# Kernel tuning notes

Hardware: AMD Instinct MI355X
Metric: run time of the kernel (lower is better)

## Reference

```python
import jax, jax.numpy as jnp
import numpy as np

ALPHA = 0.2  # leaky relu negative slope
MASK_VAL = -9e15

def setup_inputs() -> dict:
    key = jax.random.key(0)
    k1, k2, k3, k4, k5 = jax.random.split(key, 5)
    B, N, F = 8, 2048, 256
    x = jax.random.normal(k1, (B, N, F), dtype=jnp.float32)
    adj = jax.random.randint(k2, (B, N, N), 0, 2, dtype=jnp.int32)
    # params scaled down to keep activations in a sane range through 4 layers
    W0 = jax.random.normal(k3, (F, F), dtype=jnp.float32) * 0.05
    Wrest = jax.random.normal(k4, (3, F, F), dtype=jnp.float32) * 0.05
    A = jax.random.normal(k5, (4, 2 * F), dtype=jnp.float32) * 0.05
    return {"x": x, "adj": adj, "W0": W0, "Wrest": Wrest, "A": A}

def _gat_layer(h, adj, W, a):
    # h: [B,N,Fin], W: [Fin,Fout], a: [2*Fout]
    Fout = W.shape[1]
    Wh = jnp.einsum('bnf,fo->bno', h, W)  # [B,N,Fout]
    # a_input @ a decomposes: e[b,i,j] = leakyrelu(a1.Wh_i + a2.Wh_j)
    f1 = Wh @ a[:Fout]   # [B,N]
    f2 = Wh @ a[Fout:]   # [B,N]
    e = jax.nn.leaky_relu(f1[:, :, None] + f2[:, None, :], ALPHA)  # [B,N,N]
    masked = jnp.where(adj > 0, e, jnp.float32(MASK_VAL))
    att = jax.nn.softmax(masked, axis=1)  # NOTE: dim=1 as in the source
    # dropout is identity in eval mode
    return jnp.einsum('bij,bjo->bio', att, Wh)  # concat=False: no elu here

def reference(x, adj, W0, Wrest, A):
    # eval mode: all F.dropout calls are identity
    h = jax.nn.leaky_relu(_gat_layer(x, adj, W0, A[0]), ALPHA)
    for i in range(Wrest.shape[0]):
        h = jax.nn.leaky_relu(_gat_layer(h, adj, Wrest[i], A[i + 1]), ALPHA)
    return h
```

## Files before the change

### kernel.cpp

```cpp
#include <hip/hip_runtime.h>
#include <math.h>

#define BB 8
#define NN 2048
#define FF 256
#define NW 64
#define ALPHA 0.2f
#define L2E 1.44269504f

typedef _Float16 f16x8 __attribute__((ext_vector_type(8)));
typedef __fp16   h16x2 __attribute__((ext_vector_type(2)));
typedef float    f32x4 __attribute__((ext_vector_type(4)));
typedef unsigned long long u64;

__device__ __forceinline__ float lrelu(float x){ return fmaxf(x, ALPHA*x); }

__global__ void pack_prep(const int* __restrict__ adj, u64* __restrict__ packed,
                          const float* __restrict__ x, _Float16* __restrict__ h0,
                          const float* __restrict__ W0, const float* __restrict__ Wrest,
                          _Float16* __restrict__ Wt){
    __shared__ _Float16 Ls[64][66];
    int blk = blockIdx.x, t = threadIdx.x;
    if (blk < 64){
        int lw = blk >> 4, rest = blk & 15;
        int c0 = (rest >> 2)*64, k0 = (rest & 3)*64;
        const float* Win = (lw == 0) ? W0 : (Wrest + (size_t)(lw-1)*FF*FF);
        for (int it = 0; it < 4; ++it){
            int idx = it*256 + t;
            int r = idx >> 4, c4 = (idx & 15)*4;
            float4 v = *(const float4*)&Win[(size_t)(k0 + r)*FF + c0 + c4];
            Ls[c4+0][r] = (_Float16)v.x; Ls[c4+1][r] = (_Float16)v.y;
            Ls[c4+2][r] = (_Float16)v.z; Ls[c4+3][r] = (_Float16)v.w;
        }
        __syncthreads();
        int c = t >> 2, jch = t & 3;
        const unsigned* lp = (const unsigned*)&Ls[c][jch*16];
        int4 o0 = make_int4(lp[0], lp[1], lp[2], lp[3]);
        int4 o1 = make_int4(lp[4], lp[5], lp[6], lp[7]);
        _Float16* dst = Wt + ((size_t)lw*FF + c0 + c)*FF + k0 + jch*16;
        *(int4*)dst = o0;
        *(int4*)(dst + 8) = o1;
    }
    long long idx = (long long)blk*blockDim.x + t;
    long long stride = (long long)gridDim.x*blockDim.x;
    const long long total = (long long)BB*NN*NN;
    for (long long i = idx; i < total; i += stride){
        u64 m = __ballot(adj[i] > 0);
        if ((t & 63) == 0) packed[i >> 6] = m;
    }
    const long long nx4 = (long long)BB*NN*FF/4;
    for (long long i = idx; i < nx4; i += stride){
        float4 v = ((const float4*)x)[i];
        union { _Float16 h[4]; u64 u; } cv;
        cv.h[0] = (_Float16)v.x; cv.h[1] = (_Float16)v.y;
        cv.h[2] = (_Float16)v.z; cv.h[3] = (_Float16)v.w;
        ((u64*)h0)[i] = cv.u;
    }
}

__global__ __launch_bounds__(512,2) void gemm_hw(const _Float16* __restrict__ hin,
        const _Float16* __restrict__ Wt, const float* __restrict__ Avec,
        char* __restrict__ Bp, float* __restrict__ f1, float* __restrict__ f2){
    __shared__ float fred[2][64][4];
    int t = threadIdx.x, l = t & 63, wid = t >> 6;
    int wr = wid >> 2, wc = wid & 3;
    int lg = l >> 4, lr = l & 15;
    size_t i0 = (size_t)blockIdx.x * 64;
    f32x4 acc[2][4] = {};
    for (int k0 = 0; k0 < FF; k0 += 32){
        f16x8 a[2], bf[4];
        #pragma unroll
        for (int m = 0; m < 2; ++m){
            int4 v = *(const int4*)&hin[(i0 + wr*32 + m*16 + lr)*FF + k0 + lg*8];
            a[m] = *(f16x8*)&v;
        }
        #pragma unroll
        for (int n = 0; n < 4; ++n){
            int4 v = *(const int4*)&Wt[(size_t)(wc*64 + n*16 + lr)*FF + k0 + lg*8];
            bf[n] = *(f16x8*)&v;
        }
        #pragma unroll
        for (int m = 0; m < 2; ++m)
            #pragma unroll
            for (int n = 0; n < 4; ++n)
                acc[m][n] = __builtin_amdgcn_mfma_f32_16x16x32_f16(a[m], bf[n], acc[m][n], 0, 0, 0);
    }
    int b   = (int)(i0 >> 11);
    int i0l = (int)(i0 & (NN-1));
    char* Bpb = Bp + ((size_t)b << 20);
    int kb  = (i0l >> 5) + wr;
    #pragma unroll
    for (int m = 0; m < 2; ++m){
        int lgp = m*2 + (lg >> 1);
        int eb  = (lg & 1)*4;
        #pragma unroll
        for (int n = 0; n < 4; ++n){
            union { _Float16 h[4]; u64 u; } pk;
            pk.h[0] = (_Float16)acc[m][n][0]; pk.h[1] = (_Float16)acc[m][n][1];
            pk.h[2] = (_Float16)acc[m][n][2]; pk.h[3] = (_Float16)acc[m][n][3];
            int c16 = wc*4 + n;
            size_t off = ((size_t)(c16*64 + kb) << 10) + (size_t)((lgp*16 + lr)*16 + eb*2);
            *(u64*)(Bpb + off) = pk.u;
        }
    }
    float a1v[4], a2v[4];
    #pragma unroll
    for (int n = 0; n < 4; ++n){
        a1v[n] = Avec[wc*64 + n*16 + lr];
        a2v[n] = Avec[FF + wc*64 + n*16 + lr];
    }
    #pragma unroll
    for (int m = 0; m < 2; ++m){
        #pragma unroll
        for (int q = 0; q < 4; ++q){
            float p1 = 0.f, p2 = 0.f;
            #pragma unroll
            for (int n = 0; n < 4; ++n){
                float v = acc[m][n][q];
                p1 = fmaf(v, a1v[n], p1);
                p2 = fmaf(v, a2v[n], p2);
            }
            #pragma unroll
            for (int msk = 1; msk < 16; msk <<= 1){
                p1 += __shfl_xor(p1, msk);
                p2 += __shfl_xor(p2, msk);
            }
            if (lr == 0){
                fred[0][wr*32 + m*16 + lg*4 + q][wc] = p1;
                fred[1][wr*32 + m*16 + lg*4 + q][wc] = p2;
            }
        }
    }
    __syncthreads();
    if (t < 128){
        int row = t & 63, f = t >> 6;
        float v = fred[f][row][0] + fred[f][row][1] + fred[f][row][2] + fred[f][row][3];
        (f ? f2 : f1)[i0 + row] = v * L2E;
    }
}

__global__ __launch_bounds__(512,2) void spass_g(const u64* __restrict__ packed,
        const float* __restrict__ f1, const float* __restrict__ f2, float* __restrict__ g){
    __shared__ float sred[128][33];
    __shared__ float sred2[8][33];
    int blk = blockIdx.x, t = threadIdx.x;
    int b2 = blk >> 6, jt = blk & 63;
    const unsigned* pb32 = (const unsigned*)(packed + (size_t)b2*NN*(NW/2));
    const float* f1b = f1 + b2*NN;
    int jg = t & 3, ic = t >> 2;
    int j0 = jt*32 + jg*8;
    float f2v[8];
    *(float4*)&f2v[0] = *(const float4*)&f2[b2*NN + j0];
    *(float4*)&f2v[4] = *(const float4*)&f2[b2*NN + j0 + 4];
    int wi = jt, sh = jg*8;
    float acc[8] = {};
    #pragma unroll 4
    for (int ii = 0; ii < 16; ++ii){
        int i = ic*16 + ii;
        unsigned w = pb32[(size_t)i*NW + wi] >> sh;
        float f1v = f1b[i];
        #pragma unroll
        for (int e = 0; e < 8; ++e){
            float xv = f1v + f2v[e];
            float p = __builtin_amdgcn_exp2f(fmaxf(xv, ALPHA*xv));
            acc[e] += ((w >> e) & 1u) ? p : 0.f;
        }
    }
    #pragma unroll
    for (int e = 0; e < 8; ++e) sred[ic][jg*8 + e] = acc[e];
    __syncthreads();
    if (t < 256){
        int j = t & 31, part = t >> 5;
        float s = 0.f;
        #pragma unroll
        for (int k = 0; k < 16; ++k) s += sred[part*16 + k][j];
        sred2[part][j] = s;
    }
    __syncthreads();
    if (t < 32){
        float s = 0.f;
        #pragma unroll
        for (int p = 0; p < 8; ++p) s += sred2[p][t];
        g[b2*NN + jt*32 + t] = -__builtin_amdgcn_logf(s);
    }
}

__global__ __launch_bounds__(512,2) void gemm_att(const char* __restrict__ Bp,
        const u64* __restrict__ packed64, const float* __restrict__ f1,
        const float* __restrict__ f2, const float* __restrict__ g,
        _Float16* __restrict__ hnext, float* __restrict__ out, int last){
    __shared__ char Ps0[8192];
    __shared__ char Ps1[8192];
    __shared__ float FG[2][NN];
    int t = threadIdx.x, l = t & 63, wid = t >> 6;
    int lg = l >> 4, lr = l & 15;
    int b  = blockIdx.x & 7;
    int i0 = (blockIdx.x >> 3) * 64;
    const char* Bpw = Bp + ((size_t)b << 20) + ((size_t)(wid*2*64) << 10) + (size_t)(l << 4);
    const u64* pb = packed64 + (size_t)b*NN*(NW/2);
    ((float4*)&FG[0][0])[t] = ((const float4*)(f2 + b*NN))[t];
    ((float4*)&FG[1][0])[t] = ((const float4*)(g  + b*NN))[t];
    int prow = t >> 3, pch = t & 7;
    float f1v = f1[b*NN + i0 + prow];
    const u64* prowp = pb + (size_t)(i0 + prow)*(NW/2);
    int pso = prow*128 + ((pch << 4) ^ ((prow & 7) << 4));

    int4 brega[4], bregb[4];
    float fv[8], gv[8];
    unsigned w8;
    f32x4 acc[4][2] = {};

    #define LOADB(reg_, ks_) do{                                                       \
        _Pragma("unroll")                                                              \
        for (int n = 0; n < 2; ++n)                                                    \
          _Pragma("unroll")                                                            \
          for (int kk = 0; kk < 2; ++kk)                                               \
            reg_[n*2+kk] = *(const int4*)(Bpw + (((size_t)(n*64 + (ks_)*2 + kk)) << 10)); \
    }while(0)

    #define LOADP(ks_) do{                                                             \
        w8 = (unsigned)(prowp[ks_] >> (pch*8)) & 0xffu;                                \
        int jb_ = (ks_)*64 + pch*8;                                                    \
        *(float4*)&fv[0] = *(const float4*)&FG[0][jb_];                                \
        *(float4*)&fv[4] = *(const float4*)&FG[0][jb_+4];                              \
        *(float4*)&gv[0] = *(const float4*)&FG[1][jb_];                                \
        *(float4*)&gv[4] = *(const float4*)&FG[1][jb_+4];                              \
    }while(0)

    #define WRITEP(pbase_) do{                                                         \
        float pf_[8];                                                                  \
        _Pragma("unroll")                                                              \
        for (int e = 0; e < 8; ++e){                                                   \
            float xv_ = f1v + fv[e];                                                   \
            float p_ = __builtin_amdgcn_exp2f(fmaxf(xv_, ALPHA*xv_) + gv[e]);          \
            pf_[e] = ((w8 >> e) & 1u) ? p_ : 0.f;                                      \
        }                                                                              \
        union { h16x2 h2[4]; f16x8 v8; } pu_;                                          \
        pu_.h2[0] = __builtin_amdgcn_cvt_pkrtz(pf_[0], pf_[1]);                        \
        pu_.h2[1] = __builtin_amdgcn_cvt_pkrtz(pf_[2], pf_[3]);                        \
        pu_.h2[2] = __builtin_amdgcn_cvt_pkrtz(pf_[4], pf_[5]);                        \
        pu_.h2[3] = __builtin_amdgcn_cvt_pkrtz(pf_[6], pf_[7]);                        \
        *(f16x8*)((pbase_) + pso) = pu_.v8;                                            \
    }while(0)

    #define MFMA_STEP(reg_, pbase_) do{                                                \
        f16x8 pa_[4][2];                                                               \
        _Pragma("unroll")                                                              \
        for (int m = 0; m < 4; ++m){                                                   \
            int row_ = m*16 + lr;                                                      \
            _Pragma("unroll")                                                          \
            for (int kk = 0; kk < 2; ++kk)                                             \
                pa_[m][kk] = *(const f16x8*)((pbase_) + row_*128 + (((kk*4 + lg) << 4) ^ ((row_ & 7) << 4))); \
        }                                                                              \
        _Pragma("unroll")                                                              \
        for (int n = 0; n < 2; ++n)                                                    \
          _Pragma("unroll")                                                            \
          for (int kk = 0; kk < 2; ++kk){                                              \
            f16x8 bf_ = *(const f16x8*)&reg_[n*2+kk];                                  \
            _Pragma("unroll")                                                          \
            for (int m = 0; m < 4; ++m)                                                \
                acc[m][n] = __builtin_amdgcn_mfma_f32_16x16x32_f16(pa_[m][kk], bf_, acc[m][n], 0, 0, 0); \
          }                                                                            \
    }while(0)

    LOADB(brega, 0);
    __syncthreads();
    LOADP(0); WRITEP(Ps0);
    __syncthreads();
    for (int ks2 = 0; ks2 < 16; ++ks2){
        int s = 2*ks2;
        LOADB(bregb, s+1); LOADP(s+1);
        MFMA_STEP(brega, Ps0);
        WRITEP(Ps1);
        __syncthreads();
        if (ks2 < 15){ LOADB(brega, s+2); LOADP(s+2); }
        MFMA_STEP(bregb, Ps1);
        if (ks2 < 15){ WRITEP(Ps0); __syncthreads(); }
    }
    #undef LOADB
    #undef LOADP
    #undef WRITEP
    #undef MFMA_STEP

    size_t obase = (size_t)b*NN*FF;
    #pragma unroll
    for (int m = 0; m < 4; ++m){
        #pragma unroll
        for (int q = 0; q < 4; ++q){
            size_t row = i0 + m*16 + lg*4 + q;
            #pragma unroll
            for (int n = 0; n < 2; ++n){
                int col = wid*32 + n*16 + lr;
                float v = lrelu(acc[m][n][q]);
                if (last) out[obase + row*FF + col] = v;
                else      hnext[obase + row*FF + col] = (_Float16)v;
            }
        }
    }
}

extern "C" void kernel_launch(void* const* d_in, const int* in_sizes, int n_in,
                              void* d_out, int out_size, void* d_ws, size_t ws_size,
                              hipStream_t stream){
    const float* x     = (const float*)d_in[0];
    const int*   adj   = (const int*)  d_in[1];
    const float* W0    = (const float*)d_in[2];
    const float* Wrest = (const float*)d_in[3];
    const float* A     = (const float*)d_in[4];
    float* out = (float*)d_out;

    char* ws = (char*)d_ws;
    size_t off = 0;
    auto carve = [&](size_t bytes) -> void* {
        void* p = ws + off;
        off += (bytes + 255) & ~(size_t)255;
        return p;
    };
    u64*      packed = (u64*)     carve((size_t)BB*NN*NN/8);
    _Float16* hA     = (_Float16*)carve((size_t)BB*NN*FF*2);
    _Float16* hB     = (_Float16*)carve((size_t)BB*NN*FF*2);
    char*     Bp     = (char*)    carve((size_t)BB*NN*FF*2);
    _Float16* Wt     = (_Float16*)carve((size_t)4*FF*FF*2);
    float*    f1     = (float*)   carve((size_t)BB*NN*4);
    float*    f2     = (float*)   carve((size_t)BB*NN*4);
    float*    g      = (float*)   carve((size_t)BB*NN*4);

    pack_prep<<<2048, 256, 0, stream>>>(adj, packed, x, hA, W0, Wrest, Wt);

    _Float16* bufs[2] = {hA, hB};
    const _Float16* hin = hA;
    for (int layer = 0; layer < 4; ++layer){
        const float* Al = A + (size_t)layer*2*FF;
        gemm_hw<<<256, 512, 0, stream>>>(hin, Wt + (size_t)layer*FF*FF, Al, Bp, f1, f2);
        spass_g<<<512, 512, 0, stream>>>(packed, f1, f2, g);
        int last = (layer == 3);
        _Float16* hnext = bufs[(layer + 1) & 1];
        gemm_att<<<256, 512, 0, stream>>>(Bp, packed, f1, f2, g, hnext, out, last);
        hin = hnext;
    }
}
```

Baseline: 239.6 us.

## Split gemm_hw across column halves and double gemm_att k-step per barrier

```diff
diff --git a/kernel.cpp b/kernel.cpp
--- a/kernel.cpp
+++ b/kernel.cpp
@@ -7,6 +7,7 @@
 #define NW 64
 #define ALPHA 0.2f
 #define L2E 1.44269504f
+#define BBNN (BB*NN)
 
 typedef _Float16 f16x8 __attribute__((ext_vector_type(8)));
 typedef __fp16   h16x2 __attribute__((ext_vector_type(2)));
@@ -60,29 +61,30 @@
 
 __global__ __launch_bounds__(512,2) void gemm_hw(const _Float16* __restrict__ hin,
         const _Float16* __restrict__ Wt, const float* __restrict__ Avec,
-        char* __restrict__ Bp, float* __restrict__ f1, float* __restrict__ f2){
+        char* __restrict__ Bp, float* __restrict__ f1p, float* __restrict__ f2p){
     __shared__ float fred[2][64][4];
     int t = threadIdx.x, l = t & 63, wid = t >> 6;
     int wr = wid >> 2, wc = wid & 3;
     int lg = l >> 4, lr = l & 15;
-    size_t i0 = (size_t)blockIdx.x * 64;
-    f32x4 acc[2][4] = {};
+    size_t i0 = (size_t)(blockIdx.x >> 1) * 64;
+    int chalf = blockIdx.x & 1, c0 = chalf * 128;
+    f32x4 acc[2][2] = {};
     for (int k0 = 0; k0 < FF; k0 += 32){
-        f16x8 a[2], bf[4];
+        f16x8 a[2], bf[2];
         #pragma unroll
         for (int m = 0; m < 2; ++m){
             int4 v = *(const int4*)&hin[(i0 + wr*32 + m*16 + lr)*FF + k0 + lg*8];
             a[m] = *(f16x8*)&v;
         }
         #pragma unroll
-        for (int n = 0; n < 4; ++n){
-            int4 v = *(const int4*)&Wt[(size_t)(wc*64 + n*16 + lr)*FF + k0 + lg*8];
+        for (int n = 0; n < 2; ++n){
+            int4 v = *(const int4*)&Wt[(size_t)(c0 + wc*32 + n*16 + lr)*FF + k0 + lg*8];
             bf[n] = *(f16x8*)&v;
         }
         #pragma unroll
         for (int m = 0; m < 2; ++m)
             #pragma unroll
-            for (int n = 0; n < 4; ++n)
+            for (int n = 0; n < 2; ++n)
                 acc[m][n] = __builtin_amdgcn_mfma_f32_16x16x32_f16(a[m], bf[n], acc[m][n], 0, 0, 0);
     }
     int b   = (int)(i0 >> 11);
@@ -94,20 +96,20 @@
         int lgp = m*2 + (lg >> 1);
         int eb  = (lg & 1)*4;
         #pragma unroll
-        for (int n = 0; n < 4; ++n){
+        for (int n = 0; n < 2; ++n){
             union { _Float16 h[4]; u64 u; } pk;
             pk.h[0] = (_Float16)acc[m][n][0]; pk.h[1] = (_Float16)acc[m][n][1];
             pk.h[2] = (_Float16)acc[m][n][2]; pk.h[3] = (_Float16)acc[m][n][3];
-            int c16 = wc*4 + n;
+            int c16 = chalf*8 + wc*2 + n;
             size_t off = ((size_t)(c16*64 + kb) << 10) + (size_t)((lgp*16 + lr)*16 + eb*2);
             *(u64*)(Bpb + off) = pk.u;
         }
     }
-    float a1v[4], a2v[4];
-    #pragma unroll
-    for (int n = 0; n < 4; ++n){
-        a1v[n] = Avec[wc*64 + n*16 + lr];
-        a2v[n] = Avec[FF + wc*64 + n*16 + lr];
+    float a1v[2], a2v[2];
+    #pragma unroll
+    for (int n = 0; n < 2; ++n){
+        a1v[n] = Avec[c0 + wc*32 + n*16 + lr];
+        a2v[n] = Avec[FF + c0 + wc*32 + n*16 + lr];
     }
     #pragma unroll
     for (int m = 0; m < 2; ++m){
@@ -115,7 +117,7 @@
         for (int q = 0; q < 4; ++q){
             float p1 = 0.f, p2 = 0.f;
             #pragma unroll
-            for (int n = 0; n < 4; ++n){
+            for (int n = 0; n < 2; ++n){
                 float v = acc[m][n][q];
                 p1 = fmaf(v, a1v[n], p1);
                 p2 = fmaf(v, a2v[n], p2);
@@ -135,30 +137,37 @@
     if (t < 128){
         int row = t & 63, f = t >> 6;
         float v = fred[f][row][0] + fred[f][row][1] + fred[f][row][2] + fred[f][row][3];
-        (f ? f2 : f1)[i0 + row] = v * L2E;
+        (f ? f2p : f1p)[chalf*BBNN + i0 + row] = v * L2E;
     }
 }
 
 __global__ __launch_bounds__(512,2) void spass_g(const u64* __restrict__ packed,
-        const float* __restrict__ f1, const float* __restrict__ f2, float* __restrict__ g){
+        const float* __restrict__ f1p, const float* __restrict__ f2p, float* __restrict__ g){
     __shared__ float sred[128][33];
     __shared__ float sred2[8][33];
     int blk = blockIdx.x, t = threadIdx.x;
     int b2 = blk >> 6, jt = blk & 63;
     const unsigned* pb32 = (const unsigned*)(packed + (size_t)b2*NN*(NW/2));
-    const float* f1b = f1 + b2*NN;
+    const float* f1b0 = f1p + b2*NN;
+    const float* f1b1 = f1p + BBNN + b2*NN;
     int jg = t & 3, ic = t >> 2;
     int j0 = jt*32 + jg*8;
     float f2v[8];
-    *(float4*)&f2v[0] = *(const float4*)&f2[b2*NN + j0];
-    *(float4*)&f2v[4] = *(const float4*)&f2[b2*NN + j0 + 4];
+    {
+        float4 a0 = *(const float4*)&f2p[b2*NN + j0];
+        float4 a1 = *(const float4*)&f2p[b2*NN + j0 + 4];
+        float4 b0 = *(const float4*)&f2p[BBNN + b2*NN + j0];
+        float4 b1 = *(const float4*)&f2p[BBNN + b2*NN + j0 + 4];
+        f2v[0]=a0.x+b0.x; f2v[1]=a0.y+b0.y; f2v[2]=a0.z+b0.z; f2v[3]=a0.w+b0.w;
+        f2v[4]=a1.x+b1.x; f2v[5]=a1.y+b1.y; f2v[6]=a1.z+b1.z; f2v[7]=a1.w+b1.w;
+    }
     int wi = jt, sh = jg*8;
     float acc[8] = {};
     #pragma unroll 4
     for (int ii = 0; ii < 16; ++ii){
         int i = ic*16 + ii;
         unsigned w = pb32[(size_t)i*NW + wi] >> sh;
-        float f1v = f1b[i];
+        float f1v = f1b0[i] + f1b1[i];
         #pragma unroll
         for (int e = 0; e < 8; ++e){
             float xv = f1v + f2v[e];
@@ -186,11 +195,11 @@
 }
 
 __global__ __launch_bounds__(512,2) void gemm_att(const char* __restrict__ Bp,
-        const u64* __restrict__ packed64, const float* __restrict__ f1,
-        const float* __restrict__ f2, const float* __restrict__ g,
+        const u64* __restrict__ packed64, const float* __restrict__ f1p,
+        const float* __restrict__ f2p, const float* __restrict__ g,
         _Float16* __restrict__ hnext, float* __restrict__ out, int last){
-    __shared__ char Ps0[8192];
-    __shared__ char Ps1[8192];
+    __shared__ char Ps0[16384];
+    __shared__ char Ps1[16384];
     __shared__ float FG[2][NN];
     int t = threadIdx.x, l = t & 63, wid = t >> 6;
     int lg = l >> 4, lr = l & 15;
@@ -198,68 +207,92 @@
     int i0 = (blockIdx.x >> 3) * 64;
     const char* Bpw = Bp + ((size_t)b << 20) + ((size_t)(wid*2*64) << 10) + (size_t)(l << 4);
     const u64* pb = packed64 + (size_t)b*NN*(NW/2);
-    ((float4*)&FG[0][0])[t] = ((const float4*)(f2 + b*NN))[t];
-    ((float4*)&FG[1][0])[t] = ((const float4*)(g  + b*NN))[t];
+    {
+        float4 a = ((const float4*)(f2p + b*NN))[t];
+        float4 c = ((const float4*)(f2p + BBNN + b*NN))[t];
+        float4 s; s.x=a.x+c.x; s.y=a.y+c.y; s.z=a.z+c.z; s.w=a.w+c.w;
+        ((float4*)&FG[0][0])[t] = s;
+        ((float4*)&FG[1][0])[t] = ((const float4*)(g + b*NN))[t];
+    }
     int prow = t >> 3, pch = t & 7;
-    float f1v = f1[b*NN + i0 + prow];
+    int grow = b*NN + i0 + prow;
+    float f1v = f1p[grow] + f1p[BBNN + grow];
     const u64* prowp = pb + (size_t)(i0 + prow)*(NW/2);
-    int pso = prow*128 + ((pch << 4) ^ ((prow & 7) << 4));
-
-    int4 brega[4], bregb[4];
-    float fv[8], gv[8];
-    unsigned w8;
+    int psrow = prow*256;
+    int swz = (prow & 7) << 4;
+    int psoA = psrow + ((pch << 4) ^ swz);
+    int psoB = psrow + (((8 + pch) << 4) ^ swz);
+
+    int4 brega[8], bregb[8];
+    float fva[8], gva[8], fvb[8], gvb[8];
+    unsigned w8a, w8b;
     f32x4 acc[4][2] = {};
 
-    #define LOADB(reg_, ks_) do{                                                       \
+    #define LOADB(reg_, KS_) do{                                                       \
         _Pragma("unroll")                                                              \
         for (int n = 0; n < 2; ++n)                                                    \
           _Pragma("unroll")                                                            \
-          for (int kk = 0; kk < 2; ++kk)                                               \
-            reg_[n*2+kk] = *(const int4*)(Bpw + (((size_t)(n*64 + (ks_)*2 + kk)) << 10)); \
+          for (int kk = 0; kk < 4; ++kk)                                               \
+            reg_[n*4+kk] = *(const int4*)(Bpw + (((size_t)(n*64 + (KS_)*4 + kk)) << 10)); \
     }while(0)
 
-    #define LOADP(ks_) do{                                                             \
-        w8 = (unsigned)(prowp[ks_] >> (pch*8)) & 0xffu;                                \
-        int jb_ = (ks_)*64 + pch*8;                                                    \
-        *(float4*)&fv[0] = *(const float4*)&FG[0][jb_];                                \
-        *(float4*)&fv[4] = *(const float4*)&FG[0][jb_+4];                              \
-        *(float4*)&gv[0] = *(const float4*)&FG[1][jb_];                                \
-        *(float4*)&gv[4] = *(const float4*)&FG[1][jb_+4];                              \
+    #define LOADP(KS_) do{                                                             \
+        w8a = (unsigned)(prowp[(KS_)*2]   >> (pch*8)) & 0xffu;                         \
+        w8b = (unsigned)(prowp[(KS_)*2+1] >> (pch*8)) & 0xffu;                         \
+        int ja_ = (KS_)*128 + pch*8;                                                   \
+        int jb_ = ja_ + 64;                                                            \
+        *(float4*)&fva[0] = *(const float4*)&FG[0][ja_];                               \
+        *(float4*)&fva[4] = *(const float4*)&FG[0][ja_+4];                             \
+        *(float4*)&gva[0] = *(const float4*)&FG[1][ja_];                               \
+        *(float4*)&gva[4] = *(const float4*)&FG[1][ja_+4];                             \
+        *(float4*)&fvb[0] = *(const float4*)&FG[0][jb_];                               \
+        *(float4*)&fvb[4] = *(const float4*)&FG[0][jb_+4];                             \
+        *(float4*)&gvb[0] = *(const float4*)&FG[1][jb_];                               \
+        *(float4*)&gvb[4] = *(const float4*)&FG[1][jb_+4];                             \
     }while(0)
 
     #define WRITEP(pbase_) do{                                                         \
-        float pf_[8];                                                                  \
+        float pfa_[8], pfb_[8];                                                        \
         _Pragma("unroll")                                                              \
         for (int e = 0; e < 8; ++e){                                                   \
-            float xv_ = f1v + fv[e];                                                   \
-            float p_ = __builtin_amdgcn_exp2f(fmaxf(xv_, ALPHA*xv_) + gv[e]);          \
-            pf_[e] = ((w8 >> e) & 1u) ? p_ : 0.f;                                      \
+            float xa_ = f1v + fva[e];                                                  \
+            float pa2_ = __builtin_amdgcn_exp2f(fmaxf(xa_, ALPHA*xa_) + gva[e]);       \
+            pfa_[e] = ((w8a >> e) & 1u) ? pa2_ : 0.f;                                  \
+            float xb_ = f1v + fvb[e];                                                  \
+            float pb2_ = __builtin_amdgcn_exp2f(fmaxf(xb_, ALPHA*xb_) + gvb[e]);       \
+            pfb_[e] = ((w8b >> e) & 1u) ? pb2_ : 0.f;                                  \
         }                                                                              \
-        union { h16x2 h2[4]; f16x8 v8; } pu_;                                          \
-        pu_.h2[0] = __builtin_amdgcn_cvt_pkrtz(pf_[0], pf_[1]);                        \
-        pu_.h2[1] = __builtin_amdgcn_cvt_pkrtz(pf_[2], pf_[3]);                        \
-        pu_.h2[2] = __builtin_amdgcn_cvt_pkrtz(pf_[4], pf_[5]);                        \
-        pu_.h2[3] = __builtin_amdgcn_cvt_pkrtz(pf_[6], pf_[7]);                        \
-        *(f16x8*)((pbase_) + pso) = pu_.v8;                                            \
+        union { h16x2 h2[4]; f16x8 v8; } ua_, ub_;                                     \
+        ua_.h2[0] = __builtin_amdgcn_cvt_pkrtz(pfa_[0], pfa_[1]);                      \
+        ua_.h2[1] = __builtin_amdgcn_cvt_pkrtz(pfa_[2], pfa_[3]);                      \
+        ua_.h2[2] = __builtin_amdgcn_cvt_pkrtz(pfa_[4], pfa_[5]);                      \
+        ua_.h2[3] = __builtin_amdgcn_cvt_pkrtz(pfa_[6], pfa_[7]);                      \
+        ub_.h2[0] = __builtin_amdgcn_cvt_pkrtz(pfb_[0], pfb_[1]);                      \
+        ub_.h2[1] = __builtin_amdgcn_cvt_pkrtz(pfb_[2], pfb_[3]);                      \
+        ub_.h2[2] = __builtin_amdgcn_cvt_pkrtz(pfb_[4], pfb_[5]);                      \
+        ub_.h2[3] = __builtin_amdgcn_cvt_pkrtz(pfb_[6], pfb_[7]);                      \
+        *(f16x8*)((pbase_) + psoA) = ua_.v8;                                           \
+        *(f16x8*)((pbase_) + psoB) = ub_.v8;                                           \
     }while(0)
 
     #define MFMA_STEP(reg_, pbase_) do{                                                \
-        f16x8 pa_[4][2];                                                               \
         _Pragma("unroll")                                                              \
-        for (int m = 0; m < 4; ++m){                                                   \
-            int row_ = m*16 + lr;                                                      \
-            _Pragma("unroll")                                                          \
-            for (int kk = 0; kk < 2; ++kk)                                             \
-                pa_[m][kk] = *(const f16x8*)((pbase_) + row_*128 + (((kk*4 + lg) << 4) ^ ((row_ & 7) << 4))); \
-        }                                                                              \
-        _Pragma("unroll")                                                              \
-        for (int n = 0; n < 2; ++n)                                                    \
+        for (int h = 0; h < 2; ++h)                                                    \
           _Pragma("unroll")                                                            \
           for (int kk = 0; kk < 2; ++kk){                                              \
-            f16x8 bf_ = *(const f16x8*)&reg_[n*2+kk];                                  \
+            f16x8 pa_[4];                                                              \
             _Pragma("unroll")                                                          \
-            for (int m = 0; m < 4; ++m)                                                \
-                acc[m][n] = __builtin_amdgcn_mfma_f32_16x16x32_f16(pa_[m][kk], bf_, acc[m][n], 0, 0, 0); \
+            for (int m = 0; m < 4; ++m){                                               \
+                int row_ = m*16 + lr;                                                  \
+                pa_[m] = *(const f16x8*)((pbase_) + row_*256 + ((((h*8 + kk*4 + lg)) << 4) ^ ((row_ & 7) << 4))); \
+            }                                                                          \
+            _Pragma("unroll")                                                          \
+            for (int n = 0; n < 2; ++n){                                               \
+                f16x8 bf_ = *(const f16x8*)&reg_[n*4 + h*2 + kk];                      \
+                _Pragma("unroll")                                                      \
+                for (int m = 0; m < 4; ++m)                                            \
+                    acc[m][n] = __builtin_amdgcn_mfma_f32_16x16x32_f16(pa_[m], bf_, acc[m][n], 0, 0, 0); \
+            }                                                                          \
           }                                                                            \
     }while(0)
 
@@ -267,15 +300,15 @@
     __syncthreads();
     LOADP(0); WRITEP(Ps0);
     __syncthreads();
-    for (int ks2 = 0; ks2 < 16; ++ks2){
+    for (int ks2 = 0; ks2 < 8; ++ks2){
         int s = 2*ks2;
         LOADB(bregb, s+1); LOADP(s+1);
         MFMA_STEP(brega, Ps0);
         WRITEP(Ps1);
         __syncthreads();
-        if (ks2 < 15){ LOADB(brega, s+2); LOADP(s+2); }
+        if (ks2 < 7){ LOADB(brega, s+2); LOADP(s+2); }
         MFMA_STEP(bregb, Ps1);
-        if (ks2 < 15){ WRITEP(Ps0); __syncthreads(); }
+        if (ks2 < 7){ WRITEP(Ps0); __syncthreads(); }
     }
     #undef LOADB
     #undef LOADP
@@ -321,9 +354,9 @@
     _Float16* hB     = (_Float16*)carve((size_t)BB*NN*FF*2);
     char*     Bp     = (char*)    carve((size_t)BB*NN*FF*2);
     _Float16* Wt     = (_Float16*)carve((size_t)4*FF*FF*2);
-    float*    f1     = (float*)   carve((size_t)BB*NN*4);
-    float*    f2     = (float*)   carve((size_t)BB*NN*4);
-    float*    g      = (float*)   carve((size_t)BB*NN*4);
+    float*    f1p    = (float*)   carve((size_t)2*BBNN*4);
+    float*    f2p    = (float*)   carve((size_t)2*BBNN*4);
+    float*    g      = (float*)   carve((size_t)BBNN*4);
 
     pack_prep<<<2048, 256, 0, stream>>>(adj, packed, x, hA, W0, Wrest, Wt);
 
@@ -331,11 +364,11 @@
     const _Float16* hin = hA;
     for (int layer = 0; layer < 4; ++layer){
         const float* Al = A + (size_t)layer*2*FF;
-        gemm_hw<<<256, 512, 0, stream>>>(hin, Wt + (size_t)layer*FF*FF, Al, Bp, f1, f2);
-        spass_g<<<512, 512, 0, stream>>>(packed, f1, f2, g);
+        gemm_hw<<<512, 512, 0, stream>>>(hin, Wt + (size_t)layer*FF*FF, Al, Bp, f1p, f2p);
+        spass_g<<<512, 512, 0, stream>>>(packed, f1p, f2p, g);
         int last = (layer == 3);
         _Float16* hnext = bufs[(layer + 1) & 1];
-        gemm_att<<<256, 512, 0, stream>>>(Bp, packed, f1, f2, g, hnext, out, last);
+        gemm_att<<<256, 512, 0, stream>>>(Bp, packed, f1p, f2p, g, hnext, out, last);
         hin = hnext;
     }
 }
```

Measured after the change: 257.0 us. 7.3% more time.

## Fuse next layer's feature GEMM and attention projections into attention kernel

Applied to the files above, without the earlier changes.

```diff
diff --git a/kernel.cpp b/kernel.cpp
--- a/kernel.cpp
+++ b/kernel.cpp
@@ -7,6 +7,7 @@
 #define NW 64
 #define ALPHA 0.2f
 #define L2E 1.44269504f
+#define BBNN (BB*NN)
 
 typedef _Float16 f16x8 __attribute__((ext_vector_type(8)));
 typedef __fp16   h16x2 __attribute__((ext_vector_type(2)));
@@ -185,10 +186,200 @@
     }
 }
 
-__global__ __launch_bounds__(512,2) void gemm_att(const char* __restrict__ Bp,
+__global__ __launch_bounds__(512,2) void att_hw(const char* __restrict__ Bp_in,
+        char* __restrict__ Bp_out, const u64* __restrict__ packed64,
+        const float* __restrict__ f1_in, const float* __restrict__ f2_in,
+        const float* __restrict__ g, const _Float16* __restrict__ Wt,
+        const float* __restrict__ Avec, float* __restrict__ f1_out, float* __restrict__ f2_out){
+    __shared__ __align__(16) char SM[34816];
+    char* Ps0 = SM;
+    char* Ps1 = SM + 8192;
+    float* FG0 = (float*)(SM + 16384);
+    float* FG1 = FG0 + NN;
+    int t = threadIdx.x, l = t & 63, wid = t >> 6;
+    int lg = l >> 4, lr = l & 15;
+    int b  = blockIdx.x & 7;
+    int i0 = (blockIdx.x >> 3) * 64;
+    const char* Bpw = Bp_in + ((size_t)b << 20) + ((size_t)(wid*2*64) << 10) + (size_t)(l << 4);
+    const u64* pb = packed64 + (size_t)b*NN*(NW/2);
+    ((float4*)FG0)[t] = ((const float4*)(f2_in + b*NN))[t];
+    ((float4*)FG1)[t] = ((const float4*)(g + b*NN))[t];
+    int prow = t >> 3, pch = t & 7;
+    float f1v = f1_in[b*NN + i0 + prow];
+    const u64* prowp = pb + (size_t)(i0 + prow)*(NW/2);
+    int pso = prow*128 + ((pch << 4) ^ ((prow & 7) << 4));
+
+    int4 brega[4], bregb[4];
+    float fv[8], gv[8];
+    unsigned w8;
+    f32x4 acc[4][2] = {};
+
+    #define LOADB(reg_, ks_) do{                                                       \
+        _Pragma("unroll")                                                              \
+        for (int n = 0; n < 2; ++n)                                                    \
+          _Pragma("unroll")                                                            \
+          for (int kk = 0; kk < 2; ++kk)                                               \
+            reg_[n*2+kk] = *(const int4*)(Bpw + (((size_t)(n*64 + (ks_)*2 + kk)) << 10)); \
+    }while(0)
+
+    #define LOADP(ks_) do{                                                             \
+        w8 = (unsigned)(prowp[ks_] >> (pch*8)) & 0xffu;                                \
+        int jb_ = (ks_)*64 + pch*8;                                                    \
+        *(float4*)&fv[0] = *(const float4*)&FG0[jb_];                                  \
+        *(float4*)&fv[4] = *(const float4*)&FG0[jb_+4];                                \
+        *(float4*)&gv[0] = *(const float4*)&FG1[jb_];                                  \
+        *(float4*)&gv[4] = *(const float4*)&FG1[jb_+4];                                \
+    }while(0)
+
+    #define WRITEP(pbase_) do{                                                         \
+        float pf_[8];                                                                  \
+        _Pragma("unroll")                                                              \
+        for (int e = 0; e < 8; ++e){                                                   \
+            float xv_ = f1v + fv[e];                                                   \
+            float p_ = __builtin_amdgcn_exp2f(fmaxf(xv_, ALPHA*xv_) + gv[e]);          \
+            pf_[e] = ((w8 >> e) & 1u) ? p_ : 0.f;                                      \
+        }                                                                              \
+        union { h16x2 h2[4]; f16x8 v8; } pu_;                                          \
+        pu_.h2[0] = __builtin_amdgcn_cvt_pkrtz(pf_[0], pf_[1]);                        \
+        pu_.h2[1] = __builtin_amdgcn_cvt_pkrtz(pf_[2], pf_[3]);                        \
+        pu_.h2[2] = __builtin_amdgcn_cvt_pkrtz(pf_[4], pf_[5]);                        \
+        pu_.h2[3] = __builtin_amdgcn_cvt_pkrtz(pf_[6], pf_[7]);                        \
+        *(f16x8*)((pbase_) + pso) = pu_.v8;                                            \
+    }while(0)
+
+    #define MFMA_STEP(reg_, pbase_) do{                                                \
+        f16x8 pa_[4][2];                                                               \
+        _Pragma("unroll")                                                              \
+        for (int m = 0; m < 4; ++m){                                                   \
+            int row_ = m*16 + lr;                                                      \
+            _Pragma("unroll")                                                          \
+            for (int kk = 0; kk < 2; ++kk)                                             \
+                pa_[m][kk] = *(const f16x8*)((pbase_) + row_*128 + (((kk*4 + lg) << 4) ^ ((row_ & 7) << 4))); \
+        }                                                                              \
+        _Pragma("unroll")                                                              \
+        for (int n = 0; n < 2; ++n)                                                    \
+          _Pragma("unroll")                                                            \
+          for (int kk = 0; kk < 2; ++kk){                                              \
+            f16x8 bf_ = *(const f16x8*)&reg_[n*2+kk];                                  \
+            _Pragma("unroll")                                                          \
+            for (int m = 0; m < 4; ++m)                                                \
+                acc[m][n] = __builtin_amdgcn_mfma_f32_16x16x32_f16(pa_[m][kk], bf_, acc[m][n], 0, 0, 0); \
+          }                                                                            \
+    }while(0)
+
+    LOADB(brega, 0);
+    __syncthreads();
+    LOADP(0); WRITEP(Ps0);
+    __syncthreads();
+    for (int ks2 = 0; ks2 < 16; ++ks2){
+        int s = 2*ks2;
+        LOADB(bregb, s+1); LOADP(s+1);
+        MFMA_STEP(brega, Ps0);
+        WRITEP(Ps1);
+        __syncthreads();
+        if (ks2 < 15){ LOADB(brega, s+2); LOADP(s+2); }
+        MFMA_STEP(bregb, Ps1);
+        if (ks2 < 15){ WRITEP(Ps0); __syncthreads(); }
+    }
+    #undef LOADB
+    #undef LOADP
+    #undef WRITEP
+    #undef MFMA_STEP
+
+    __syncthreads();
+    #pragma unroll
+    for (int m = 0; m < 4; ++m){
+        #pragma unroll
+        for (int q = 0; q < 4; ++q){
+            int row = m*16 + lg*4 + q;
+            #pragma unroll
+            for (int n = 0; n < 2; ++n){
+                int col = wid*32 + n*16 + lr;
+                float v = lrelu(acc[m][n][q]);
+                *(_Float16*)(SM + row*512 + ((col*2) ^ ((row & 7) << 4))) = (_Float16)v;
+            }
+        }
+    }
+    __syncthreads();
+
+    {
+        float (*fred)[64][4] = (float(*)[64][4])(SM + 32768);
+        int wr = wid >> 2, wc = wid & 3;
+        f32x4 acc2[2][4] = {};
+        for (int k0 = 0; k0 < FF; k0 += 32){
+            f16x8 a[2], bf[4];
+            #pragma unroll
+            for (int m = 0; m < 2; ++m){
+                int row = wr*32 + m*16 + lr;
+                a[m] = *(const f16x8*)(SM + row*512 + (((k0 + lg*8)*2) ^ ((row & 7) << 4)));
+            }
+            #pragma unroll
+            for (int n = 0; n < 4; ++n){
+                int4 v = *(const int4*)&Wt[(size_t)(wc*64 + n*16 + lr)*FF + k0 + lg*8];
+                bf[n] = *(f16x8*)&v;
+            }
+            #pragma unroll
+            for (int m = 0; m < 2; ++m)
+                #pragma unroll
+                for (int n = 0; n < 4; ++n)
+                    acc2[m][n] = __builtin_amdgcn_mfma_f32_16x16x32_f16(a[m], bf[n], acc2[m][n], 0, 0, 0);
+        }
+        char* Bpb = Bp_out + ((size_t)b << 20);
+        int kb = (i0 >> 5) + wr;
+        #pragma unroll
+        for (int m = 0; m < 2; ++m){
+            int lgp = m*2 + (lg >> 1);
+            int eb  = (lg & 1)*4;
+            #pragma unroll
+            for (int n = 0; n < 4; ++n){
+                union { _Float16 h[4]; u64 u; } pk;
+                pk.h[0] = (_Float16)acc2[m][n][0]; pk.h[1] = (_Float16)acc2[m][n][1];
+                pk.h[2] = (_Float16)acc2[m][n][2]; pk.h[3] = (_Float16)acc2[m][n][3];
+                int c16 = wc*4 + n;
+                size_t off = ((size_t)(c16*64 + kb) << 10) + (size_t)((lgp*16 + lr)*16 + eb*2);
+                *(u64*)(Bpb + off) = pk.u;
+            }
+        }
+        float a1v[4], a2v[4];
+        #pragma unroll
+        for (int n = 0; n < 4; ++n){
+            a1v[n] = Avec[wc*64 + n*16 + lr];
+            a2v[n] = Avec[FF + wc*64 + n*16 + lr];
+        }
+        #pragma unroll
+        for (int m = 0; m < 2; ++m){
+            #pragma unroll
+            for (int q = 0; q < 4; ++q){
+                float p1 = 0.f, p2 = 0.f;
+                #pragma unroll
+                for (int n = 0; n < 4; ++n){
+                    float v = acc2[m][n][q];
+                    p1 = fmaf(v, a1v[n], p1);
+                    p2 = fmaf(v, a2v[n], p2);
+                }
+                #pragma unroll
+                for (int msk = 1; msk < 16; msk <<= 1){
+                    p1 += __shfl_xor(p1, msk);
+                    p2 += __shfl_xor(p2, msk);
+                }
+                if (lr == 0){
+                    fred[0][wr*32 + m*16 + lg*4 + q][wc] = p1;
+                    fred[1][wr*32 + m*16 + lg*4 + q][wc] = p2;
+                }
+            }
+        }
+        __syncthreads();
+        if (t < 128){
+            int row = t & 63, f = t >> 6;
+            float v = fred[f][row][0] + fred[f][row][1] + fred[f][row][2] + fred[f][row][3];
+            (f ? f2_out : f1_out)[b*NN + i0 + row] = v * L2E;
+        }
+    }
+}
+
+__global__ __launch_bounds__(512,2) void att_last(const char* __restrict__ Bp,
         const u64* __restrict__ packed64, const float* __restrict__ f1,
-        const float* __restrict__ f2, const float* __restrict__ g,
-        _Float16* __restrict__ hnext, float* __restrict__ out, int last){
+        const float* __restrict__ f2, const float* __restrict__ g, float* __restrict__ out){
     __shared__ char Ps0[8192];
     __shared__ char Ps1[8192];
     __shared__ float FG[2][NN];
@@ -291,9 +482,7 @@
             #pragma unroll
             for (int n = 0; n < 2; ++n){
                 int col = wid*32 + n*16 + lr;
-                float v = lrelu(acc[m][n][q]);
-                if (last) out[obase + row*FF + col] = v;
-                else      hnext[obase + row*FF + col] = (_Float16)v;
+                out[obase + row*FF + col] = lrelu(acc[m][n][q]);
             }
         }
     }
@@ -318,24 +507,28 @@
     };
     u64*      packed = (u64*)     carve((size_t)BB*NN*NN/8);
     _Float16* hA     = (_Float16*)carve((size_t)BB*NN*FF*2);
-    _Float16* hB     = (_Float16*)carve((size_t)BB*NN*FF*2);
-    char*     Bp     = (char*)    carve((size_t)BB*NN*FF*2);
+    char*     Bp0    = (char*)    carve((size_t)BB*NN*FF*2);
+    char*     Bp1    = (char*)    carve((size_t)BB*NN*FF*2);
     _Float16* Wt     = (_Float16*)carve((size_t)4*FF*FF*2);
-    float*    f1     = (float*)   carve((size_t)BB*NN*4);
-    float*    f2     = (float*)   carve((size_t)BB*NN*4);
-    float*    g      = (float*)   carve((size_t)BB*NN*4);
+    float*    f1a    = (float*)   carve((size_t)BBNN*4);
+    float*    f2a    = (float*)   carve((size_t)BBNN*4);
+    float*    f1b    = (float*)   carve((size_t)BBNN*4);
+    float*    f2b    = (float*)   carve((size_t)BBNN*4);
+    float*    g      = (float*)   carve((size_t)BBNN*4);
+
+    float* f1s[2] = {f1a, f1b};
+    float* f2s[2] = {f2a, f2b};
+    char*  Bps[2] = {Bp0, Bp1};
 
     pack_prep<<<2048, 256, 0, stream>>>(adj, packed, x, hA, W0, Wrest, Wt);
-
-    _Float16* bufs[2] = {hA, hB};
-    const _Float16* hin = hA;
-    for (int layer = 0; layer < 4; ++layer){
-        const float* Al = A + (size_t)layer*2*FF;
-        gemm_hw<<<256, 512, 0, stream>>>(hin, Wt + (size_t)layer*FF*FF, Al, Bp, f1, f2);
-        spass_g<<<512, 512, 0, stream>>>(packed, f1, f2, g);
-        int last = (layer == 3);
-        _Float16* hnext = bufs[(layer + 1) & 1];
-        gemm_att<<<256, 512, 0, stream>>>(Bp, packed, f1, f2, g, hnext, out, last);
-        hin = hnext;
-    }
+    gemm_hw<<<256, 512, 0, stream>>>(hA, Wt, A, Bp0, f1a, f2a);
+    for (int lyr = 0; lyr < 3; ++lyr){
+        spass_g<<<512, 512, 0, stream>>>(packed, f1s[lyr & 1], f2s[lyr & 1], g);
+        att_hw<<<256, 512, 0, stream>>>(Bps[lyr & 1], Bps[(lyr + 1) & 1], packed,
+                                        f1s[lyr & 1], f2s[lyr & 1], g,
+                                        Wt + (size_t)(lyr + 1)*FF*FF, A + (size_t)(lyr + 1)*2*FF,
+                                        f1s[(lyr + 1) & 1], f2s[(lyr + 1) & 1]);
+    }
+    spass_g<<<512, 512, 0, stream>>>(packed, f1s[1], f2s[1], g);
+    att_last<<<256, 512, 0, stream>>>(Bps[1], packed, f1s[1], f2s[1], g, out);
 }
```

Measured after the change: 212.3 us. 1.13x faster.
